# Kernel optimization log

Hardware: AMD Instinct MI355X
Metric: run time of the kernel (lower is better)

The kernel has to match this reference:

```python
import jax, jax.numpy as jnp
import numpy as np
from jax import lax

VOCAB = 32000
D = 64
B = 32
S = 512
DECAY_P = 0.1  # p in rho_t = (1-p)*rho_{t-1} + outer(x_t, x_t)


def setup_inputs() -> dict:
    key = jax.random.key(0)
    k1, k2 = jax.random.split(key)
    x = jax.random.randint(k1, (B, S), 0, VOCAB, dtype=jnp.int64)
    emb = jax.random.normal(k2, (VOCAB, D), dtype=jnp.float32)
    return {"x": x, "emb": emb}


def reference(x, emb):
    # Embedding lookup: [B, S, D]
    content = emb[x]
    # Per-token outer products (projectedRho): [B, S, D, D]
    proj = jnp.einsum('bsi,bsj->bsij', content, content)
    # Initial rho = identity, repeated over batch: [B, D, D]
    init_rho = jnp.broadcast_to(jnp.eye(D, dtype=emb.dtype), (B, D, D))
    decay = jnp.asarray(1.0 - DECAY_P, dtype=emb.dtype)

    def step(rho, p_t):
        rho = rho * decay + p_t  # [B, D, D]
        return rho, rho

    # scan over time axis; proj transposed to [S, B, D, D]
    _, states = lax.scan(step, init_rho, jnp.swapaxes(proj, 0, 1))
    # states: [S, B, D, D] -> return as [B, S, D, D] (stacked list of states)
    return jnp.swapaxes(states, 0, 1)
```

## Files before the change

kernel.cpp:

```cpp
#include <hip/hip_runtime.h>

#define VOCAB 32000
#define D     64
#define B     32
#define S     512
#define NCHUNK 16
#define CLEN   32

typedef float vf4 __attribute__((ext_vector_type(4)));

#define DECAY  0.9f
#define DECAYC 0.034336838202925312f

__global__ void qmn_gather(const int* __restrict__ x,
                           const vf4* __restrict__ emb4,
                           vf4* __restrict__ content4) {
    int tid = blockIdx.x * blockDim.x + threadIdx.x;
    int bs  = tid >> 4;
    int d4  = tid & 15;
    int tok = x[bs];
    content4[tid] = emb4[tok * (D / 4) + d4];
}

__global__ __launch_bounds__(256, 4) void qmn_partial(
    const float* __restrict__ content,
    vf4*        __restrict__ P4)
{
    int blk   = blockIdx.x;
    int c     = blk & 15;
    int b     = (blk >> 4) & 31;
    int iBase = (blk >> 9) * 16;

    int jq = threadIdx.x & 15;
    int i  = iBase + (threadIdx.x >> 4);

    const float* cb  = content + (size_t)b * S * D;
    const vf4*   cb4 = (const vf4*)cb;
    const int    t0  = c * CLEN;

    vf4 acc; acc.x = 0.f; acc.y = 0.f; acc.z = 0.f; acc.w = 0.f;

    #pragma unroll 8
    for (int tt = 0; tt < CLEN; ++tt) {
        int t = t0 + tt;
        float ci = cb[t * D + i];
        vf4   cj = cb4[t * (D / 4) + jq];
        acc.x = acc.x * DECAY + ci * cj.x;
        acc.y = acc.y * DECAY + ci * cj.y;
        acc.z = acc.z * DECAY + ci * cj.z;
        acc.w = acc.w * DECAY + ci * cj.w;
    }

    P4[(((b * NCHUNK + c) * D) + i) * (D / 4) + jq] = acc;
}

__global__ __launch_bounds__(256) void qmn_prefix(
    const vf4* __restrict__ P4,
    vf4*       __restrict__ R4)
{
    int tid = blockIdx.x * 256 + threadIdx.x;
    int jq  = tid & 15;
    int i   = (tid >> 4) & 63;
    int b   = tid >> 10;

    vf4 r;
    int j0 = jq * 4;
    r.x = (i == j0 + 0) ? 1.0f : 0.0f;
    r.y = (i == j0 + 1) ? 1.0f : 0.0f;
    r.z = (i == j0 + 2) ? 1.0f : 0.0f;
    r.w = (i == j0 + 3) ? 1.0f : 0.0f;

    const vf4* Pb  = P4 + (size_t)b * NCHUNK * D * (D / 4);
    vf4*       Rb  = R4 + (size_t)b * NCHUNK * D * (D / 4);
    const int  off = i * (D / 4) + jq;

    Rb[off] = r;

    #pragma unroll
    for (int c = 1; c < NCHUNK; ++c) {
        vf4 p = Pb[(c - 1) * D * (D / 4) + off];
        r.x = r.x * DECAYC + p.x;
        r.y = r.y * DECAYC + p.y;
        r.z = r.z * DECAYC + p.z;
        r.w = r.w * DECAYC + p.w;
        Rb[c * D * (D / 4) + off] = r;
    }
}

__global__ __launch_bounds__(256, 8) void qmn_store(
    const float* __restrict__ content,
    const vf4*  __restrict__ R4,
    vf4*        __restrict__ out4)
{
    __shared__ vf4 lds4[CLEN * D / 4];
    float* ldsf = (float*)lds4;

    int blk   = blockIdx.x;
    int c     = blk & 15;
    int b     = (blk >> 4) & 31;
    int iBase = (blk >> 9) * 16;

    int jq = threadIdx.x & 15;
    int i  = iBase + (threadIdx.x >> 4);

    const int tStart = c * CLEN;

    const vf4* cb4 = (const vf4*)(content + (size_t)b * S * D);
    #pragma unroll
    for (int k = 0; k < CLEN * D / 4 / 256; ++k) {
        int idx = k * 256 + threadIdx.x;
        lds4[idx] = cb4[tStart * (D / 4) + idx];
    }

    vf4 rho = R4[(((b * NCHUNK + c) * D) + i) * (D / 4) + jq];

    __syncthreads();

    vf4* outp = out4 + (((size_t)(b * S + tStart)) * D + i) * (D / 4) + jq;

    #pragma unroll 4
    for (int tt = 0; tt < CLEN; ++tt) {
        float ci = ldsf[tt * D + i];
        vf4   cj = lds4[tt * (D / 4) + jq];
        rho.x = rho.x * DECAY + ci * cj.x;
        rho.y = rho.y * DECAY + ci * cj.y;
        rho.z = rho.z * DECAY + ci * cj.z;
        rho.w = rho.w * DECAY + ci * cj.w;
        __builtin_nontemporal_store(rho, outp);
        outp += D * (D / 4);
    }
}

extern "C" void kernel_launch(void* const* d_in, const int* in_sizes, int n_in,
                              void* d_out, int out_size, void* d_ws, size_t ws_size,
                              hipStream_t stream) {
    const int*   x   = (const int*)d_in[0];
    const float* emb = (const float*)d_in[1];
    vf4* out = (vf4*)d_out;

    float* content = (float*)d_ws;
    vf4*   P4 = (vf4*)((char*)d_ws + (size_t)B * S * D * sizeof(float));
    vf4*   R4 = (vf4*)((char*)d_ws + (size_t)B * S * D * sizeof(float)
                                   + (size_t)B * NCHUNK * D * D * sizeof(float));

    qmn_gather<<<B * S * (D / 4) / 256, 256, 0, stream>>>(
        x, (const vf4*)emb, (vf4*)content);

    qmn_partial<<<B * NCHUNK * 4, 256, 0, stream>>>(content, P4);

    qmn_prefix<<<(B * D * 16) / 256, 256, 0, stream>>>(P4, R4);

    qmn_store<<<B * NCHUNK * 4, 256, 0, stream>>>(content, R4, out);
}
```

Baseline: 304.7 us.

## Fuse embedding gather and chunk prefix into partial and store kernels

Removes the separate gather kernel and prefix kernel, leaving two launches. Each block gathers its chunk's embeddings straight from the table into LDS. The store kernel rebuilds the chunk-start state by serially combining the earlier chunk partials itself. This cuts two launches and the workspace round-trips for content and R. In exchange, the partial sums are re-read redundantly, up to 15 per block in later chunks, and both kernels repeat the embedding gather.

```diff
diff --git a/kernel.cpp b/kernel.cpp
--- a/kernel.cpp
+++ b/kernel.cpp
@@ -12,85 +12,11 @@
 #define DECAY  0.9f
 #define DECAYC 0.034336838202925312f
 
-__global__ void qmn_gather(const int* __restrict__ x,
-                           const vf4* __restrict__ emb4,
-                           vf4* __restrict__ content4) {
-    int tid = blockIdx.x * blockDim.x + threadIdx.x;
-    int bs  = tid >> 4;
-    int d4  = tid & 15;
-    int tok = x[bs];
-    content4[tid] = emb4[tok * (D / 4) + d4];
-}
 
-__global__ __launch_bounds__(256, 4) void qmn_partial(
-    const float* __restrict__ content,
-    vf4*        __restrict__ P4)
-{
-    int blk   = blockIdx.x;
-    int c     = blk & 15;
-    int b     = (blk >> 4) & 31;
-    int iBase = (blk >> 9) * 16;
-
-    int jq = threadIdx.x & 15;
-    int i  = iBase + (threadIdx.x >> 4);
-
-    const float* cb  = content + (size_t)b * S * D;
-    const vf4*   cb4 = (const vf4*)cb;
-    const int    t0  = c * CLEN;
-
-    vf4 acc; acc.x = 0.f; acc.y = 0.f; acc.z = 0.f; acc.w = 0.f;
-
-    #pragma unroll 8
-    for (int tt = 0; tt < CLEN; ++tt) {
-        int t = t0 + tt;
-        float ci = cb[t * D + i];
-        vf4   cj = cb4[t * (D / 4) + jq];
-        acc.x = acc.x * DECAY + ci * cj.x;
-        acc.y = acc.y * DECAY + ci * cj.y;
-        acc.z = acc.z * DECAY + ci * cj.z;
-        acc.w = acc.w * DECAY + ci * cj.w;
-    }
-
-    P4[(((b * NCHUNK + c) * D) + i) * (D / 4) + jq] = acc;
-}
-
-__global__ __launch_bounds__(256) void qmn_prefix(
-    const vf4* __restrict__ P4,
-    vf4*       __restrict__ R4)
-{
-    int tid = blockIdx.x * 256 + threadIdx.x;
-    int jq  = tid & 15;
-    int i   = (tid >> 4) & 63;
-    int b   = tid >> 10;
-
-    vf4 r;
-    int j0 = jq * 4;
-    r.x = (i == j0 + 0) ? 1.0f : 0.0f;
-    r.y = (i == j0 + 1) ? 1.0f : 0.0f;
-    r.z = (i == j0 + 2) ? 1.0f : 0.0f;
-    r.w = (i == j0 + 3) ? 1.0f : 0.0f;
-
-    const vf4* Pb  = P4 + (size_t)b * NCHUNK * D * (D / 4);
-    vf4*       Rb  = R4 + (size_t)b * NCHUNK * D * (D / 4);
-    const int  off = i * (D / 4) + jq;
-
-    Rb[off] = r;
-
-    #pragma unroll
-    for (int c = 1; c < NCHUNK; ++c) {
-        vf4 p = Pb[(c - 1) * D * (D / 4) + off];
-        r.x = r.x * DECAYC + p.x;
-        r.y = r.y * DECAYC + p.y;
-        r.z = r.z * DECAYC + p.z;
-        r.w = r.w * DECAYC + p.w;
-        Rb[c * D * (D / 4) + off] = r;
-    }
-}
-
-__global__ __launch_bounds__(256, 8) void qmn_store(
-    const float* __restrict__ content,
-    const vf4*  __restrict__ R4,
-    vf4*        __restrict__ out4)
+__global__ __launch_bounds__(256, 8) void qmn_partial(
+    const int* __restrict__ x,
+    const vf4* __restrict__ emb4,
+    vf4*       __restrict__ P4)
 {
     __shared__ vf4 lds4[CLEN * D / 4];
     float* ldsf = (float*)lds4;
@@ -102,17 +28,71 @@
 
     int jq = threadIdx.x & 15;
     int i  = iBase + (threadIdx.x >> 4);
-
     const int tStart = c * CLEN;
 
-    const vf4* cb4 = (const vf4*)(content + (size_t)b * S * D);
     #pragma unroll
-    for (int k = 0; k < CLEN * D / 4 / 256; ++k) {
+    for (int k = 0; k < CLEN * (D / 4) / 256; ++k) {
         int idx = k * 256 + threadIdx.x;
-        lds4[idx] = cb4[tStart * (D / 4) + idx];
+        int tok = x[b * S + tStart + (idx >> 4)];
+        lds4[idx] = emb4[tok * (D / 4) + (idx & 15)];
+    }
+    __syncthreads();
+
+    vf4 acc; acc.x = 0.f; acc.y = 0.f; acc.z = 0.f; acc.w = 0.f;
+
+    #pragma unroll
+    for (int tt = 0; tt < CLEN; ++tt) {
+        float ci = ldsf[tt * D + i];
+        vf4   cj = lds4[tt * (D / 4) + jq];
+        acc.x = acc.x * DECAY + ci * cj.x;
+        acc.y = acc.y * DECAY + ci * cj.y;
+        acc.z = acc.z * DECAY + ci * cj.z;
+        acc.w = acc.w * DECAY + ci * cj.w;
     }
 
-    vf4 rho = R4[(((b * NCHUNK + c) * D) + i) * (D / 4) + jq];
+    P4[(((b * NCHUNK + c) * D) + i) * (D / 4) + jq] = acc;
+}
+
+__global__ __launch_bounds__(256, 8) void qmn_store(
+    const int* __restrict__ x,
+    const vf4* __restrict__ emb4,
+    const vf4* __restrict__ P4,
+    vf4*       __restrict__ out4)
+{
+    __shared__ vf4 lds4[CLEN * D / 4];
+    float* ldsf = (float*)lds4;
+
+    int blk   = blockIdx.x;
+    int c     = blk & 15;
+    int b     = (blk >> 4) & 31;
+    int iBase = (blk >> 9) * 16;
+
+    int jq = threadIdx.x & 15;
+    int i  = iBase + (threadIdx.x >> 4);
+    const int tStart = c * CLEN;
+
+    #pragma unroll
+    for (int k = 0; k < CLEN * (D / 4) / 256; ++k) {
+        int idx = k * 256 + threadIdx.x;
+        int tok = x[b * S + tStart + (idx >> 4)];
+        lds4[idx] = emb4[tok * (D / 4) + (idx & 15)];
+    }
+
+    vf4 rho;
+    int j0 = jq * 4;
+    rho.x = (i == j0 + 0) ? 1.0f : 0.0f;
+    rho.y = (i == j0 + 1) ? 1.0f : 0.0f;
+    rho.z = (i == j0 + 2) ? 1.0f : 0.0f;
+    rho.w = (i == j0 + 3) ? 1.0f : 0.0f;
+
+    const vf4* Pb = P4 + ((size_t)b * NCHUNK * D) * (D / 4) + i * (D / 4) + jq;
+    for (int k = 0; k < c; ++k) {
+        vf4 p = Pb[k * D * (D / 4)];
+        rho.x = rho.x * DECAYC + p.x;
+        rho.y = rho.y * DECAYC + p.y;
+        rho.z = rho.z * DECAYC + p.z;
+        rho.w = rho.w * DECAYC + p.w;
+    }
 
     __syncthreads();
 
@@ -138,17 +118,11 @@
     const float* emb = (const float*)d_in[1];
     vf4* out = (vf4*)d_out;
 
-    float* content = (float*)d_ws;
-    vf4*   P4 = (vf4*)((char*)d_ws + (size_t)B * S * D * sizeof(float));
-    vf4*   R4 = (vf4*)((char*)d_ws + (size_t)B * S * D * sizeof(float)
-                                   + (size_t)B * NCHUNK * D * D * sizeof(float));
+    vf4* P4 = (vf4*)d_ws;
 
-    qmn_gather<<<B * S * (D / 4) / 256, 256, 0, stream>>>(
-        x, (const vf4*)emb, (vf4*)content);
+    qmn_partial<<<B * NCHUNK * 4, 256, 0, stream>>>(
+        x, (const vf4*)emb, P4);
 
-    qmn_partial<<<B * NCHUNK * 4, 256, 0, stream>>>(content, P4);
-
-    qmn_prefix<<<(B * D * 16) / 256, 256, 0, stream>>>(P4, R4);
-
-    qmn_store<<<B * NCHUNK * 4, 256, 0, stream>>>(content, R4, out);
+    qmn_store<<<B * NCHUNK * 4, 256, 0, stream>>>(
+        x, (const vf4*)emb, P4, out);
 }
```

After: 292.8 us. 1.04x faster.
